# Kernel optimization log

Measured on AMD Instinct MI355X. Metric: run time of the kernel, lower is better.

Reference implementation:

```python
import jax, jax.numpy as jnp
import numpy as np

STRIDES = [8, 16, 32, 64, 128]
CLASS_NUM = 80
SCORE_THR = 0.05
IOU_THR = 0.6
MAX_DET = 1000


def setup_inputs() -> dict:
    key = jax.random.key(0)
    ks = jax.random.split(key, 16)
    B, H, W = 8, 1024, 1024
    inp = {}
    for i, s in enumerate(STRIDES):
        h, w = H // s, W // s
        inp[f"cls_p{i+3}"] = jax.random.normal(ks[i], (B, CLASS_NUM, h, w), jnp.float32)
        inp[f"cnt_p{i+3}"] = jax.random.normal(ks[5 + i], (B, 1, h, w), jnp.float32)
        # ltrb offsets are positive distances; scale by stride for realistic boxes
        inp[f"reg_p{i+3}"] = jax.random.uniform(ks[10 + i], (B, 4, h, w), jnp.float32) * (4.0 * s)
    inp["batch_imgs"] = jax.random.normal(ks[15], (B, 3, H, W), jnp.float32)
    return inp


def _reshape_cat(levels):
    # [B,c,h,w] -> [B,sum(h*w),c], matching permute(0,2,3,1).reshape
    B, c = levels[0].shape[0], levels[0].shape[1]
    return jnp.concatenate([jnp.transpose(p, (0, 2, 3, 1)).reshape(B, -1, c) for p in levels], axis=1)


def _coords(levels):
    cs = []
    for p, s in zip(levels, STRIDES):
        h, w = p.shape[2], p.shape[3]
        sx = jnp.arange(w, dtype=jnp.float32) * s
        sy = jnp.arange(h, dtype=jnp.float32) * s
        yy, xx = jnp.meshgrid(sy, sx, indexing='ij')
        cs.append(jnp.stack([xx.ravel(), yy.ravel()], axis=-1) + s // 2)
    return jnp.concatenate(cs, axis=0)  # [sum(h*w),2]


def _nms_keep(boxes, scores, classes, valid, iou_thr):
    # boxes [M,4] already sorted by descending score; greedy class-offset NMS
    maxc = jnp.max(boxes)
    off = classes.astype(boxes.dtype) * (maxc + 1.0)
    b = boxes + off[:, None]
    x1, y1, x2, y2 = b[:, 0], b[:, 1], b[:, 2], b[:, 3]
    areas = (x2 - x1 + 1.0) * (y2 - y1 + 1.0)
    xx1 = jnp.maximum(x1[:, None], x1[None, :])
    yy1 = jnp.maximum(y1[:, None], y1[None, :])
    xx2 = jnp.minimum(x2[:, None], x2[None, :])
    yy2 = jnp.minimum(y2[:, None], y2[None, :])
    inter = jnp.maximum(xx2 - xx1, 0.0) * jnp.maximum(yy2 - yy1, 0.0)
    iou = inter / (areas[:, None] + areas[None, :] - inter)  # [M,M]
    M = boxes.shape[0]
    idx = jnp.arange(M)

    def body(i, keep):
        sup = jnp.any(keep & (iou[:, i] > iou_thr) & (idx < i))
        return keep.at[i].set(valid[i] & jnp.logical_not(sup))

    return jax.lax.fori_loop(0, M, body, jnp.zeros((M,), dtype=bool))


def reference(cls_p3, cls_p4, cls_p5, cls_p6, cls_p7,
              cnt_p3, cnt_p4, cnt_p5, cnt_p6, cnt_p7,
              reg_p3, reg_p4, reg_p5, reg_p6, reg_p7,
              batch_imgs):
    cls_levels = [cls_p3, cls_p4, cls_p5, cls_p6, cls_p7]
    cnt_levels = [cnt_p3, cnt_p4, cnt_p5, cnt_p6, cnt_p7]
    reg_levels = [reg_p3, reg_p4, reg_p5, reg_p6, reg_p7]

    cls_logits = _reshape_cat(cls_levels)     # [B,N,C]
    cnt_logits = _reshape_cat(cnt_levels)     # [B,N,1]
    reg_preds = _reshape_cat(reg_levels)      # [B,N,4]
    coords = _coords(cls_levels)              # [N,2]

    cls_preds = jax.nn.sigmoid(cls_logits)
    cnt_preds = jax.nn.sigmoid(cnt_logits)
    cls_scores = jnp.max(cls_preds, axis=-1)                    # [B,N]
    cls_classes = jnp.argmax(cls_preds, axis=-1) + 1            # [B,N]
    cls_scores = jnp.sqrt(cls_scores * cnt_preds[..., 0])       # add_centerness

    # ltrb offsets -> xyxy boxes
    boxes = jnp.concatenate([coords[None] - reg_preds[..., :2],
                             coords[None] + reg_preds[..., 2:]], axis=-1)  # [B,N,4]

    max_num = min(MAX_DET, cls_scores.shape[-1])
    topk_scores, topk_ind = jax.lax.top_k(cls_scores, max_num)             # sorted desc
    topk_classes = jnp.take_along_axis(cls_classes, topk_ind, axis=1)
    topk_boxes = jnp.take_along_axis(boxes, topk_ind[..., None], axis=1)

    valid = topk_scores >= SCORE_THR
    keep = jax.vmap(lambda b, s, c, v: _nms_keep(b, s, c, v, IOU_THR))(
        topk_boxes, topk_scores, topk_classes, valid)                      # [B,max_num]

    # ClipBoxes
    h, w = batch_imgs.shape[2], batch_imgs.shape[3]
    cb = jnp.maximum(topk_boxes, 0.0)
    xs = jnp.minimum(cb[..., 0::2], float(w - 1))
    ys = jnp.minimum(cb[..., 1::2], float(h - 1))
    cb = jnp.stack([xs[..., 0], ys[..., 0], xs[..., 1], ys[..., 1]], axis=-1)

    scores_out = jnp.where(keep, topk_scores, 0.0)
    classes_out = jnp.where(keep, topk_classes, 0)
    boxes_out = jnp.where(keep[..., None], cb, 0.0)
    return scores_out, classes_out, boxes_out
```

## Files before the change

kernel.cpp:

```cpp
#include <hip/hip_runtime.h>
#include <stdint.h>

#define NLOC   21824
#define NQUAD  5456
#define BATCH  8
#define MAXDET 1000
#define NCLS   80

struct LevelPtrs {
    const float* cls[5];
    const float* cnt[5];
    const float* reg[5];
};

__global__ __launch_bounds__(256) void k_stage1(LevelPtrs lp, float* scores,
                                                int* cls_out, float4* boxes) {
    __shared__ float4 bl4[8][32];
    __shared__ int4   bc4[8][32];
    int tid = threadIdx.x;
    int p   = tid >> 5;
    int qq  = tid & 31;
    int blk = blockIdx.x;
    int b   = blockIdx.y;

    int lvl, qoff, logw, strd;
    if (blk < 128)      { lvl = 0; qoff = 0;    logw = 7; strd = 8;   }
    else if (blk < 160) { lvl = 1; qoff = 4096; logw = 6; strd = 16;  }
    else if (blk < 168) { lvl = 2; qoff = 5120; logw = 5; strd = 32;  }
    else if (blk < 170) { lvl = 3; qoff = 5376; logw = 4; strd = 64;  }
    else                { lvl = 4; qoff = 5440; logw = 3; strd = 128; }

    int quad  = blk * 32 + qq;
    bool valid = quad < NQUAD;
    int ql   = quad - qoff;
    int loc  = ql * 4;
    int hw   = 1 << (2 * logw);
    int hw4  = hw >> 2;

    float bl[4] = {-3.0e38f, -3.0e38f, -3.0e38f, -3.0e38f};
    int   bc[4] = {0, 0, 0, 0};
    if (valid) {
        const float4* cp = (const float4*)(lp.cls[lvl] + (size_t)(b * NCLS) * hw + loc);
        int c0 = p * 10;
#pragma unroll
        for (int g = 0; g < 2; ++g) {
            float4 lv[5];
#pragma unroll
            for (int k = 0; k < 5; ++k)
                lv[k] = cp[(size_t)(c0 + g * 5 + k) * hw4];
#pragma unroll
            for (int k = 0; k < 5; ++k) {
                int c = c0 + g * 5 + k;
                const float* lf = (const float*)&lv[k];
#pragma unroll
                for (int u = 0; u < 4; ++u)
                    if (lf[u] > bl[u]) { bl[u] = lf[u]; bc[u] = c; }
            }
        }
    }
    bl4[p][qq] = make_float4(bl[0], bl[1], bl[2], bl[3]);
    bc4[p][qq] = make_int4(bc[0], bc[1], bc[2], bc[3]);
    __syncthreads();

    if (tid < 32 && valid) {
        int q = tid;
        float4 B = bl4[0][q]; int4 C = bc4[0][q];
        float bestl[4] = {B.x, B.y, B.z, B.w};
        int   bestc[4] = {C.x, C.y, C.z, C.w};
#pragma unroll
        for (int pp = 1; pp < 8; ++pp) {
            float4 Bp = bl4[pp][q]; int4 Cp = bc4[pp][q];
            const float* bf = (const float*)&Bp;
            const int*   cf = (const int*)&Cp;
#pragma unroll
            for (int u = 0; u < 4; ++u)
                if (bf[u] > bestl[u]) { bestl[u] = bf[u]; bestc[u] = cf[u]; }
        }

        float4 lcv = *(const float4*)(lp.cnt[lvl] + (size_t)b * hw + loc);
        const float* lc = (const float*)&lcv;

        const float4* rp = (const float4*)(lp.reg[lvl] + (size_t)(b * 4) * hw + loc);
        float4 r0v = rp[0], r1v = rp[hw4], r2v = rp[2 * hw4], r3v = rp[3 * hw4];
        const float* r0 = (const float*)&r0v;
        const float* r1 = (const float*)&r1v;
        const float* r2 = (const float*)&r2v;
        const float* r3 = (const float*)&r3v;

        int x = loc & ((1 << logw) - 1);
        int y = loc >> logw;
        float cy = (float)(y * strd + (strd >> 1));

        float sc4[4]; int cl4[4]; float4 bx4[4];
#pragma unroll
        for (int u = 0; u < 4; ++u) {
            float e = expf(-bestl[u]);
            float sig_cls = 1.0f / (1.0f + e);
            float sig_cnt = 1.0f / (1.0f + expf(-lc[u]));
            sc4[u] = sqrtf(__fmul_rn(sig_cls, sig_cnt));
            cl4[u] = bestc[u] + 1;
            float cx = (float)((x + u) * strd + (strd >> 1));
            bx4[u] = make_float4(__fsub_rn(cx, r0[u]), __fsub_rn(cy, r1[u]),
                                 __fadd_rn(cx, r2[u]), __fadd_rn(cy, r3[u]));
        }

        int o = b * NLOC + quad * 4;
        *(float4*)(scores + o) = make_float4(sc4[0], sc4[1], sc4[2], sc4[3]);
        *(int4*)(cls_out + o)  = make_int4(cl4[0], cl4[1], cl4[2], cl4[3]);
#pragma unroll
        for (int u = 0; u < 4; ++u) boxes[o + u] = bx4[u];
    }
}

#define HSTR 257

__global__ __launch_bounds__(1024) void k_select(const uint32_t* scores_u,
                                                 const float4* boxes,
                                                 const int* cls_ws,
                                                 float* topk_score, float4* gbox,
                                                 int* gcls, float4* obox,
                                                 float* areas, uint64_t* nzmask) {
    __shared__ uint32_t hist[16 * HSTR];
    __shared__ uint64_t keys[2048 + 8];
    __shared__ uint32_t prefix_sh, cnt_sh;
    __shared__ int R_sh;
    __shared__ float redmax[16];
    __shared__ float maxc_sh;

    int b = blockIdx.x, tid = threadIdx.x;
    int wid = tid >> 6, lane = tid & 63;
    if (tid < 16) nzmask[b * 16 + tid] = 0;
    if (tid == 0) cnt_sh = 0;
    const uint4* sc4 = (const uint4*)(scores_u + (size_t)b * NLOC);

    uint4 sv[6];
#pragma unroll
    for (int it = 0; it < 6; ++it) {
        int n4 = tid + it * 1024;
        sv[it] = make_uint4(0u, 0u, 0u, 0u);
        if (n4 < NQUAD) sv[it] = sc4[n4];
    }

    uint32_t prefix = 0;
    int R = MAXDET;
    uint32_t* hw_ = &hist[wid * HSTR];
    for (int d = 3; d >= 0; --d) {
        for (int i = tid; i < 16 * HSTR; i += 1024) hist[i] = 0;
        __syncthreads();
        int shl = 8 * d;
        int last = -1; uint32_t run = 0;
#pragma unroll
        for (int it = 0; it < 6; ++it) {
            if (tid + it * 1024 < NQUAD) {
                uint32_t vals[4] = {sv[it].x, sv[it].y, sv[it].z, sv[it].w};
#pragma unroll
                for (int u = 0; u < 4; ++u) {
                    uint32_t sb = vals[u];
                    bool m = (d == 3) || ((sb >> (shl + 8)) == prefix);
                    int dig = m ? (int)((sb >> shl) & 255u) : -1;
                    if (dig != last) {
                        if (last >= 0 && run) atomicAdd(&hw_[last], run);
                        last = dig; run = 0;
                    }
                    if (dig >= 0) run++;
                }
            }
        }
        if (last >= 0 && run) atomicAdd(&hw_[last], run);
        __syncthreads();

        if (tid < 64) {
            uint32_t h0 = 0, h1 = 0, h2 = 0, h3 = 0;
#pragma unroll
            for (int w = 0; w < 16; ++w) {
                const uint32_t* hp = &hist[w * HSTR + tid * 4];
                h0 += hp[0]; h1 += hp[1]; h2 += hp[2]; h3 += hp[3];
            }
            uint32_t s3 = h3;
            uint32_t s2 = h2 + s3;
            uint32_t s1 = h1 + s2;
            uint32_t s0 = h0 + s1;
            uint32_t acc = s0;
#pragma unroll
            for (int off = 1; off < 64; off <<= 1) {
                uint32_t t = __shfl_down(acc, off, 64);
                if (tid + off < 64) acc += t;
            }
            uint32_t above = acc - s0;
            uint32_t cge [4] = {above + s0, above + s1, above + s2, above + s3};
            uint32_t cge1[4] = {above + s1, above + s2, above + s3, above};
#pragma unroll
            for (int u = 0; u < 4; ++u) {
                if (cge[u] >= (uint32_t)R && cge1[u] < (uint32_t)R) {
                    prefix_sh = (prefix << 8) | (uint32_t)(tid * 4 + u);
                    R_sh = R - (int)cge1[u];
                }
            }
        }
        __syncthreads();
        prefix = prefix_sh;
        R = R_sh;
    }
    uint32_t Sstar = prefix;

#pragma unroll
    for (int it = 0; it < 6; ++it) {
        int n4 = tid + it * 1024;
        uint32_t vals[4] = {sv[it].x, sv[it].y, sv[it].z, sv[it].w};
#pragma unroll
        for (int u = 0; u < 4; ++u) {
            bool pred = (n4 < NQUAD) && (vals[u] >= Sstar);
            uint64_t msk = __ballot(pred);
            if (msk) {
                int leader = __ffsll((unsigned long long)msk) - 1;
                uint32_t base = 0;
                if (lane == leader)
                    base = atomicAdd(&cnt_sh, (uint32_t)__popcll(msk));
                base = (uint32_t)__shfl((int)base, leader, 64);
                if (pred) {
                    uint32_t pos = base +
                        (uint32_t)__popcll(msk & ((1ull << lane) - 1ull));
                    if (pos < 2048) {
                        uint32_t n = (uint32_t)(n4 * 4 + u);
                        keys[pos] = ((uint64_t)vals[u] << 32) | (uint32_t)(~n);
                    }
                }
            }
        }
    }
    __syncthreads();
    uint32_t cnt = cnt_sh > 2048u ? 2048u : cnt_sh;
    if (tid < 8) keys[cnt + tid] = 0;
    __syncthreads();

    float lmax = -3.0e38f;
    float4 v0, v1; int cl0 = 0, cl1 = 0; bool k0 = false, k1 = false;
    int rk0 = 0, rk1 = 0;
    uint64_t myk0 = 0, myk1 = 0;

    if (tid < (int)cnt) {
        myk0 = keys[tid];
        for (int j = 0; j < (int)cnt; j += 8) {
            uint64_t a0 = keys[j + 0], a1 = keys[j + 1], a2 = keys[j + 2], a3 = keys[j + 3];
            uint64_t a4 = keys[j + 4], a5 = keys[j + 5], a6 = keys[j + 6], a7 = keys[j + 7];
            rk0 += (int)(a0 > myk0) + (int)(a1 > myk0) + (int)(a2 > myk0) + (int)(a3 > myk0)
                 + (int)(a4 > myk0) + (int)(a5 > myk0) + (int)(a6 > myk0) + (int)(a7 > myk0);
        }
        if (rk0 < MAXDET) {
            uint32_t n = ~(uint32_t)myk0;
            v0 = boxes[(size_t)b * NLOC + n];
            cl0 = cls_ws[(size_t)b * NLOC + n];
            topk_score[b * MAXDET + rk0] = __uint_as_float((uint32_t)(myk0 >> 32));
            gbox[b * MAXDET + rk0] = v0;
            gcls[b * MAXDET + rk0] = cl0;
            lmax = fmaxf(fmaxf(v0.x, v0.y), fmaxf(v0.z, v0.w));
            k0 = true;
        }
    }
    if ((int)cnt > 1024 && tid + 1024 < (int)cnt) {
        myk1 = keys[tid + 1024];
        for (int j = 0; j < (int)cnt; j += 8) {
            uint64_t a0 = keys[j + 0], a1 = keys[j + 1], a2 = keys[j + 2], a3 = keys[j + 3];
            uint64_t a4 = keys[j + 4], a5 = keys[j + 5], a6 = keys[j + 6], a7 = keys[j + 7];
            rk1 += (int)(a0 > myk1) + (int)(a1 > myk1) + (int)(a2 > myk1) + (int)(a3 > myk1)
                 + (int)(a4 > myk1) + (int)(a5 > myk1) + (int)(a6 > myk1) + (int)(a7 > myk1);
        }
        if (rk1 < MAXDET) {
            uint32_t n = ~(uint32_t)myk1;
            v1 = boxes[(size_t)b * NLOC + n];
            cl1 = cls_ws[(size_t)b * NLOC + n];
            topk_score[b * MAXDET + rk1] = __uint_as_float((uint32_t)(myk1 >> 32));
            gbox[b * MAXDET + rk1] = v1;
            gcls[b * MAXDET + rk1] = cl1;
            lmax = fmaxf(lmax, fmaxf(fmaxf(v1.x, v1.y), fmaxf(v1.z, v1.w)));
            k1 = true;
        }
    }

#pragma unroll
    for (int off = 32; off > 0; off >>= 1)
        lmax = fmaxf(lmax, __shfl_down(lmax, off, 64));
    if ((tid & 63) == 0) redmax[tid >> 6] = lmax;
    __syncthreads();
    if (tid == 0) {
        float m = redmax[0];
        for (int w = 1; w < 16; ++w) m = fmaxf(m, redmax[w]);
        maxc_sh = __fadd_rn(m, 1.0f);
    }
    __syncthreads();
    float maxc1 = maxc_sh;

    if (k0) {
        float off0 = __fmul_rn((float)cl0, maxc1);
        float4 o = make_float4(__fadd_rn(v0.x, off0), __fadd_rn(v0.y, off0),
                               __fadd_rn(v0.z, off0), __fadd_rn(v0.w, off0));
        obox[b * MAXDET + rk0] = o;
        areas[b * MAXDET + rk0] =
            __fmul_rn(__fadd_rn(__fsub_rn(o.z, o.x), 1.0f),
                      __fadd_rn(__fsub_rn(o.w, o.y), 1.0f));
    }
    if (k1) {
        float off1 = __fmul_rn((float)cl1, maxc1);
        float4 o = make_float4(__fadd_rn(v1.x, off1), __fadd_rn(v1.y, off1),
                               __fadd_rn(v1.z, off1), __fadd_rn(v1.w, off1));
        obox[b * MAXDET + rk1] = o;
        areas[b * MAXDET + rk1] =
            __fmul_rn(__fadd_rn(__fsub_rn(o.z, o.x), 1.0f),
                      __fadd_rn(__fsub_rn(o.w, o.y), 1.0f));
    }
}

__global__ __launch_bounds__(256) void k_iou(const float4* obox, const float* areas,
                                             uint64_t* rows, uint64_t* nzmask) {
    __shared__ float4 ob[MAXDET];
    __shared__ float  ca[MAXDET];
    __shared__ uint64_t nzloc[16];
    int b = blockIdx.x, word = blockIdx.y, tid = threadIdx.x;
    if (tid < 16) nzloc[tid] = 0;
    for (int r = tid; r < MAXDET; r += 256) {
        ob[r] = obox[b * MAXDET + r];
        ca[r] = areas[b * MAXDET + r];
    }
    __syncthreads();

    int j0 = word * 64;
    int jlim = MAXDET - j0;
    if (jlim > 64) jlim = 64;

#pragma unroll
    for (int qr = 0; qr < 4; ++qr) {
        int i = tid + qr * 256;
        if (i >= MAXDET) continue;
        uint64_t rw = 0;
        int jmax = j0 + jlim;
        if (i < jmax - 1) {
            float4 bi = ob[i];
            float ai = ca[i];
            for (int jj = 0; jj < jlim; ++jj) {
                int j = j0 + jj;
                float4 bj = ob[j0 + jj];
                float xx1 = fmaxf(bi.x, bj.x), yy1 = fmaxf(bi.y, bj.y);
                float xx2 = fminf(bi.z, bj.z), yy2 = fminf(bi.w, bj.w);
                float w_ = fmaxf(__fsub_rn(xx2, xx1), 0.0f);
                float h_ = fmaxf(__fsub_rn(yy2, yy1), 0.0f);
                float inter = __fmul_rn(w_, h_);
                float denom = __fsub_rn(__fadd_rn(ai, ca[j0 + jj]), inter);
                bool sup = (j > i) && (inter > __fmul_rn(0.6f, denom));
                rw |= sup ? (1ull << jj) : 0ull;
            }
        }
        rows[((size_t)(b * MAXDET) + i) * 16 + word] = rw;
        if (rw) atomicOr(&nzloc[i >> 6], 1ull << (i & 63));
    }
    __syncthreads();
    if (tid < 16 && nzloc[tid])
        atomicOr(&nzmask[b * 16 + tid], nzloc[tid]);
}

#define NZSTG 448

__global__ __launch_bounds__(256) void k_nms_out(const uint64_t* rows,
                                                 const uint64_t* nzmask,
                                                 const float* topk_score,
                                                 const int* gcls, const float4* gbox,
                                                 float* out) {
    __shared__ uint64_t validmask[16];
    __shared__ uint64_t keepmask[16];
    __shared__ int zlist[MAXDET];
    __shared__ int m_sh;
    __shared__ uint64_t srow[NZSTG * 16];
    int b = blockIdx.x, tid = threadIdx.x;

    if (tid < 16) validmask[tid] = 0;
    if (tid == 0) m_sh = 0;
    __syncthreads();
    for (int r = tid; r < MAXDET; r += 256)
        if (topk_score[b * MAXDET + r] >= 0.05f)
            atomicOr(&validmask[r >> 6], 1ull << (r & 63));
    if (tid < 16) {
        uint64_t nz = nzmask[b * 16 + tid];
        int cw = __popcll(nz);
        int pre = cw;
#pragma unroll
        for (int off = 1; off < 16; off <<= 1) {
            int t = __shfl_up(pre, off, 64);
            if (tid >= off) pre += t;
        }
        int base = pre - cw;
        while (nz) {
            int bit = __ffsll((unsigned long long)nz) - 1;
            nz &= nz - 1;
            zlist[base++] = tid * 64 + bit;
        }
        if (tid == 15) m_sh = base;
    }
    __syncthreads();

    int m = m_sh;
    int ms = m < NZSTG ? m : NZSTG;
    const uint64_t* rg = rows + (size_t)b * MAXDET * 16;

    for (int idx = tid; idx < ms * 16; idx += 256)
        srow[idx] = rg[(size_t)zlist[idx >> 4] * 16 + (idx & 15)];
    __syncthreads();

    uint64_t S = 0, V = 0;
    if (tid < 16) V = validmask[tid];
    if (tid < 64) {
        uint64_t row_nxt = 0;
        if (m > 0 && tid < 16)
            row_nxt = (0 < ms) ? srow[tid] : rg[(size_t)zlist[0] * 16 + tid];
        for (int k = 0; k < m; ++k) {
            uint64_t row_cur = row_nxt;
            int kn = k + 1;
            if (kn < m && tid < 16)
                row_nxt = (kn < ms) ? srow[kn * 16 + tid]
                                    : rg[(size_t)zlist[kn] * 16 + tid];
            int z = zlist[k];
            int w = z >> 6, bp = z & 63;
            uint32_t aliveV = ((uint32_t)(V >> bp) & ~(uint32_t)(S >> bp)) & 1u;
            uint32_t alive = (uint32_t)__builtin_amdgcn_readlane((int)aliveV, w);
            if (alive) S |= row_cur;
        }
    }
    if (tid < 16) keepmask[tid] = V & ~S;
    __syncthreads();

    for (int r = tid; r < MAXDET; r += 256) {
        bool keep = ((keepmask[r >> 6] >> (r & 63)) & 1ull) != 0;
        float sc = topk_score[b * MAXDET + r];
        int cl = gcls[b * MAXDET + r];
        float4 v = gbox[b * MAXDET + r];
        float c0 = fminf(fmaxf(v.x, 0.0f), 1023.0f);
        float c1 = fminf(fmaxf(v.y, 0.0f), 1023.0f);
        float c2 = fminf(fmaxf(v.z, 0.0f), 1023.0f);
        float c3 = fminf(fmaxf(v.w, 0.0f), 1023.0f);
        out[b * MAXDET + r] = keep ? sc : 0.0f;
        out[BATCH * MAXDET + b * MAXDET + r] = keep ? (float)cl : 0.0f;
        float4* op = (float4*)(out + 2 * BATCH * MAXDET) + (b * MAXDET + r);
        *op = keep ? make_float4(c0, c1, c2, c3) : make_float4(0.f, 0.f, 0.f, 0.f);
    }
}

extern "C" void kernel_launch(void* const* d_in, const int* in_sizes, int n_in,
                              void* d_out, int out_size, void* d_ws, size_t ws_size,
                              hipStream_t stream) {
    (void)in_sizes; (void)n_in; (void)out_size; (void)ws_size;

    LevelPtrs lp;
    for (int i = 0; i < 5; ++i) {
        lp.cls[i] = (const float*)d_in[3 * i + 0];
        lp.cnt[i] = (const float*)d_in[3 * i + 1];
        lp.reg[i] = (const float*)d_in[3 * i + 2];
    }

    char* ws = (char*)d_ws;
    float*    scores   = (float*)   (ws + 0);
    int*      cls_ws   = (int*)     (ws + 698368);
    float4*   boxes    = (float4*)  (ws + 1396736);
    float*    topk_sc  = (float*)   (ws + 4222208);
    int*      gcls     = (int*)     (ws + 4254208);
    float4*   gbox     = (float4*)  (ws + 4286208);
    float4*   obox     = (float4*)  (ws + 4414208);
    float*    areas    = (float*)   (ws + 4542208);
    uint64_t* rows     = (uint64_t*)(ws + 4574208);
    uint64_t* nzmask   = (uint64_t*)(ws + 5598208);

    dim3 g1(171, BATCH);
    k_stage1<<<g1, 256, 0, stream>>>(lp, scores, cls_ws, boxes);

    k_select<<<BATCH, 1024, 0, stream>>>((const uint32_t*)scores, boxes, cls_ws,
                                         topk_sc, gbox, gcls, obox, areas, nzmask);

    dim3 g4(BATCH, 16);
    k_iou<<<g4, 256, 0, stream>>>(obox, areas, rows, nzmask);

    k_nms_out<<<BATCH, 256, 0, stream>>>(rows, nzmask, topk_sc, gcls, gbox,
                                         (float*)d_out);
}
```

Before: 255.6 us.

## Replace O(n^2) rank counting with shared-memory bitonic sort in top-k select

Swaps the all-pairs rank computation over up to 2048 candidate keys for an in-shared-memory bitonic sort of 2048 zero-padded 64-bit keys, so each thread reads its sorted slot directly. This removes the quadratic comparison loop, which costs up to about 2048 LDS reads per thread, and replaces it with 66 synchronized compare-exchange passes. Keys are zeroed at kernel start so empty slots sort to the end. Validity is now signalled by a nonzero key rather than a computed rank.

Result: no change. 259.0 us (+1.4%).

```diff
diff --git a/kernel.cpp b/kernel.cpp
--- a/kernel.cpp
+++ b/kernel.cpp
@@ -121,7 +121,7 @@
                                                  int* gcls, float4* obox,
                                                  float* areas, uint64_t* nzmask) {
     __shared__ uint32_t hist[16 * HSTR];
-    __shared__ uint64_t keys[2048 + 8];
+    __shared__ uint64_t keys[2048];
     __shared__ uint32_t prefix_sh, cnt_sh;
     __shared__ int R_sh;
     __shared__ float redmax[16];
@@ -131,6 +131,8 @@
     int wid = tid >> 6, lane = tid & 63;
     if (tid < 16) nzmask[b * 16 + tid] = 0;
     if (tid == 0) cnt_sh = 0;
+    keys[tid] = 0;
+    keys[tid + 1024] = 0;
     const uint4* sc4 = (const uint4*)(scores_u + (size_t)b * NLOC);
 
     uint4 sv[6];
@@ -229,52 +231,39 @@
         }
     }
     __syncthreads();
-    uint32_t cnt = cnt_sh > 2048u ? 2048u : cnt_sh;
-    if (tid < 8) keys[cnt + tid] = 0;
-    __syncthreads();
+
+    for (int kk = 2; kk <= 2048; kk <<= 1) {
+        for (int j = kk >> 1; j > 0; j >>= 1) {
+#pragma unroll
+            for (int h = 0; h < 2; ++h) {
+                int idx = tid + h * 1024;
+                int ixj = idx ^ j;
+                if (ixj > idx) {
+                    uint64_t a  = keys[idx];
+                    uint64_t bb = keys[ixj];
+                    bool desc = ((idx & kk) == 0);
+                    if (desc ? (a < bb) : (a > bb)) {
+                        keys[idx] = bb;
+                        keys[ixj] = a;
+                    }
+                }
+            }
+            __syncthreads();
+        }
+    }
 
     float lmax = -3.0e38f;
-    float4 v0, v1; int cl0 = 0, cl1 = 0; bool k0 = false, k1 = false;
-    int rk0 = 0, rk1 = 0;
-    uint64_t myk0 = 0, myk1 = 0;
-
-    if (tid < (int)cnt) {
-        myk0 = keys[tid];
-        for (int j = 0; j < (int)cnt; j += 8) {
-            uint64_t a0 = keys[j + 0], a1 = keys[j + 1], a2 = keys[j + 2], a3 = keys[j + 3];
-            uint64_t a4 = keys[j + 4], a5 = keys[j + 5], a6 = keys[j + 6], a7 = keys[j + 7];
-            rk0 += (int)(a0 > myk0) + (int)(a1 > myk0) + (int)(a2 > myk0) + (int)(a3 > myk0)
-                 + (int)(a4 > myk0) + (int)(a5 > myk0) + (int)(a6 > myk0) + (int)(a7 > myk0);
-        }
-        if (rk0 < MAXDET) {
-            uint32_t n = ~(uint32_t)myk0;
-            v0 = boxes[(size_t)b * NLOC + n];
-            cl0 = cls_ws[(size_t)b * NLOC + n];
-            topk_score[b * MAXDET + rk0] = __uint_as_float((uint32_t)(myk0 >> 32));
-            gbox[b * MAXDET + rk0] = v0;
-            gcls[b * MAXDET + rk0] = cl0;
-            lmax = fmaxf(fmaxf(v0.x, v0.y), fmaxf(v0.z, v0.w));
-            k0 = true;
-        }
-    }
-    if ((int)cnt > 1024 && tid + 1024 < (int)cnt) {
-        myk1 = keys[tid + 1024];
-        for (int j = 0; j < (int)cnt; j += 8) {
-            uint64_t a0 = keys[j + 0], a1 = keys[j + 1], a2 = keys[j + 2], a3 = keys[j + 3];
-            uint64_t a4 = keys[j + 4], a5 = keys[j + 5], a6 = keys[j + 6], a7 = keys[j + 7];
-            rk1 += (int)(a0 > myk1) + (int)(a1 > myk1) + (int)(a2 > myk1) + (int)(a3 > myk1)
-                 + (int)(a4 > myk1) + (int)(a5 > myk1) + (int)(a6 > myk1) + (int)(a7 > myk1);
-        }
-        if (rk1 < MAXDET) {
-            uint32_t n = ~(uint32_t)myk1;
-            v1 = boxes[(size_t)b * NLOC + n];
-            cl1 = cls_ws[(size_t)b * NLOC + n];
-            topk_score[b * MAXDET + rk1] = __uint_as_float((uint32_t)(myk1 >> 32));
-            gbox[b * MAXDET + rk1] = v1;
-            gcls[b * MAXDET + rk1] = cl1;
-            lmax = fmaxf(lmax, fmaxf(fmaxf(v1.x, v1.y), fmaxf(v1.z, v1.w)));
-            k1 = true;
-        }
+    float4 v0; int cl0 = 0; bool k0 = false;
+    uint64_t myk = (tid < MAXDET) ? keys[tid] : 0;
+    if (myk) {
+        uint32_t n = ~(uint32_t)myk;
+        v0 = boxes[(size_t)b * NLOC + n];
+        cl0 = cls_ws[(size_t)b * NLOC + n];
+        topk_score[b * MAXDET + tid] = __uint_as_float((uint32_t)(myk >> 32));
+        gbox[b * MAXDET + tid] = v0;
+        gcls[b * MAXDET + tid] = cl0;
+        lmax = fmaxf(fmaxf(v0.x, v0.y), fmaxf(v0.z, v0.w));
+        k0 = true;
     }
 
 #pragma unroll
@@ -294,17 +283,8 @@
         float off0 = __fmul_rn((float)cl0, maxc1);
         float4 o = make_float4(__fadd_rn(v0.x, off0), __fadd_rn(v0.y, off0),
                                __fadd_rn(v0.z, off0), __fadd_rn(v0.w, off0));
-        obox[b * MAXDET + rk0] = o;
-        areas[b * MAXDET + rk0] =
-            __fmul_rn(__fadd_rn(__fsub_rn(o.z, o.x), 1.0f),
-                      __fadd_rn(__fsub_rn(o.w, o.y), 1.0f));
-    }
-    if (k1) {
-        float off1 = __fmul_rn((float)cl1, maxc1);
-        float4 o = make_float4(__fadd_rn(v1.x, off1), __fadd_rn(v1.y, off1),
-                               __fadd_rn(v1.z, off1), __fadd_rn(v1.w, off1));
-        obox[b * MAXDET + rk1] = o;
-        areas[b * MAXDET + rk1] =
+        obox[b * MAXDET + tid] = o;
+        areas[b * MAXDET + tid] =
             __fmul_rn(__fadd_rn(__fsub_rn(o.z, o.x), 1.0f),
                       __fadd_rn(__fsub_rn(o.w, o.y), 1.0f));
     }
```
